# Optimization experiments

Measured on AMD Instinct MI355X. Metric: run time of the kernel, lower is better.

Reference implementation:

```python
import jax, jax.numpy as jnp
import numpy as np

N, H, DK, DV, DFF, D = 2, 8, 32, 32, 512, 256
B, S = 2, 2048
MASK_VALUE = -1e-30
EPS = 1e-14  # K.epsilon()**2 with default epsilon 1e-7


def glorot(key, shape):
    fan_in, fan_out = shape[-2], shape[-1]
    limit = np.sqrt(6.0 / (fan_in + fan_out))
    return jax.random.uniform(key, shape, jnp.float32, -limit, limit)


def setup_inputs() -> dict:
    key = jax.random.key(0)
    ks = jax.random.split(key, 8)
    return {
        "x": jax.random.normal(ks[0], (B, S, D), jnp.float32),
        "mask": jnp.ones((B, S), jnp.float32),
        "Wq": glorot(ks[1], (N, H, D, DK)),
        "Wk": glorot(ks[2], (N, H, D, DK)),
        "Wv": glorot(ks[3], (N, H, D, DV)),
        "Wo": glorot(ks[4], (N, H * DV, D)),
        "W1": glorot(ks[5], (N, D, DFF)),
        "b1": jnp.zeros((N, DFF), jnp.float32),
        "W2": glorot(ks[6], (N, DFF, D)),
        "b2": jnp.zeros((N, D), jnp.float32),
        "gamma": jnp.ones((2 * N,), jnp.float32),
        "beta": jnp.zeros((2 * N,), jnp.float32),
    }


def _layernorm(x, g, b):
    mean = jnp.mean(x, axis=-1, keepdims=True)
    var = jnp.mean(jnp.square(x - mean), axis=-1, keepdims=True)
    return (x - mean) / jnp.sqrt(var + EPS) * g + b


def reference(x, mask, Wq, Wk, Wv, Wo, W1, b1, W2, b2, gamma, beta):
    m = mask[:, None, None, :]  # [B,1,1,S], multiplies score rows' key axis
    for i in range(N):
        # batched multi-head attention (no 1/sqrt(dk) scaling, faithful to source)
        q = jnp.einsum("bsd,hdk->bhsk", x, Wq[i])
        k = jnp.einsum("bsd,hdk->bhsk", x, Wk[i])
        v = jnp.einsum("bsd,hdv->bhsv", x, Wv[i])
        A = jnp.einsum("bhsk,bhtk->bhst", q, k)  # [B,H,S,S]
        A = m * A + (1.0 - m) * MASK_VALUE
        A = jax.nn.softmax(A, axis=-1)
        o = jnp.einsum("bhst,bhtv->bhsv", A, v)
        conc = o.transpose(0, 2, 1, 3).reshape(x.shape[0], x.shape[1], H * DV)
        x = x + conc @ Wo[i]
        x = _layernorm(x, gamma[2 * i], beta[2 * i])
        ffn = jax.nn.relu(x @ W1[i] + b1[i]) @ W2[i] + b2[i]
        x = x + ffn
        x = _layernorm(x, gamma[2 * i + 1], beta[2 * i + 1])
    return x
```

## Files before the change

### kernel.cpp

```cpp
#include <hip/hip_runtime.h>
#include <hip/hip_bf16.h>

#define NL 2
#define NH 8
#define DKk 32
#define DVv 32
#define DFF 512
#define DD 256
#define BB 2
#define SS 2048
#define MROWS (BB*SS)
#define MASK_VALUE (-1e-30f)
#define LN_EPS 1e-14f
#define L2E 1.4426950408889634f
#define SOFT_SHIFT_L2E (50.0f*L2E)

typedef __hip_bfloat16 bf16;
typedef unsigned short us;
typedef short bf16x8 __attribute__((ext_vector_type(8)));
typedef float f32x4  __attribute__((ext_vector_type(4)));
typedef unsigned short us4 __attribute__((ext_vector_type(4)));

#define O_XF   256
#define O_QB   (O_XF+1048576)
#define O_KH   (O_QB+1048576)
#define O_KL   (O_KH+524288)
#define O_VT   (O_KL+524288)
#define O_XH   (O_VT+524288)
#define O_XL   (O_XH+524288)
#define O_OP   (O_XL+524288)
#define O_ML   (O_OP+2097152)
#define O_MASK (O_ML+65536)
#define O_WQ   (O_MASK+4096)
#define O_WK   (O_WQ+131072)
#define O_WV   (O_WK+131072)
#define O_WO   (O_WV+131072)
#define O_W1   (O_WO+131072)
#define O_B1   (O_W1+262144)
#define O_W2   (O_B1+1024)
#define O_B2   (O_W2+262144)
#define O_GM   (O_B2+512)
#define O_BT   (O_GM+4)
#define O_PREP (O_BT+4)
#define CONV_TOTAL (1048576+4096+131072+131072+131072+131072+262144+1024+262144+512+4+4)
#define CONV_BLOCKS ((CONV_TOTAL+255)/256)
#define PQH 0u
#define PQL 393216u
#define POH 786432u
#define POL 917504u
#define P1H 1048576u
#define P1L 1310720u
#define P2H 1572864u
#define P2L 1835008u

__device__ __forceinline__ float us2f(us u){
  unsigned int v = ((unsigned int)u) << 16; float f;
  __builtin_memcpy(&f, &v, 4); return f;
}
__device__ __forceinline__ us f2bf_rne(float f){
  unsigned int b = __float_as_uint(f);
  b += 0x7FFFu + ((b>>16)&1u);
  return (us)(b>>16);
}

#if __has_builtin(__builtin_amdgcn_exp2f)
#define EXP2F(x) __builtin_amdgcn_exp2f(x)
#else
#define EXP2F(x) exp2f(x)
#endif

#if __has_builtin(__builtin_amdgcn_cvt_pk_bf16_f32)
typedef __bf16 bf16x2_t __attribute__((ext_vector_type(2)));
__device__ __forceinline__ int pack_bf16(float a, float b){
  bf16x2_t r = __builtin_amdgcn_cvt_pk_bf16_f32(a, b);
  int i; __builtin_memcpy(&i, &r, 4); return i;
}
#else
__device__ __forceinline__ int pack_bf16(float a, float b){
  int b0 = __float_as_int(a) + 0x8000;
  int b1 = __float_as_int(b) + 0x8000;
  return (b1 & 0xFFFF0000) | ((int)((unsigned)b0 >> 16));
}
#endif

__device__ __forceinline__ void gl_lds16(const us* g, us* l){
  __builtin_amdgcn_global_load_lds(
    (const __attribute__((address_space(1))) unsigned int*)g,
    (__attribute__((address_space(3))) unsigned int*)l, 16, 0, 0);
}

__device__ __forceinline__ size_t xhl_idx(int row, int col){
  int rt = row>>6, rg = (row>>4)&3, L15 = row&15;
  int kc = col>>5, Q = (col>>3)&3, j = col&7;
  return ((size_t)(rt*8+kc))*2048 + rg*512 + Q*128 + L15*8 + j;
}

__global__ void detect_kernel(const us* __restrict__ x, int n, int* __restrict__ flagp){
  __shared__ int bad;
  if(threadIdx.x==0) bad = 0;
  __syncthreads();
  int lim = n < 4096 ? n : 4096;
  int mybad = 0;
  for(int i=threadIdx.x; i<lim; i+=256){
    float f = us2f(x[i]);
    if(!(fabsf(f) < 1e3f)) mybad = 1;
  }
  if(mybad) atomicOr(&bad, 1);
  __syncthreads();
  if(threadIdx.x==0) *flagp = bad ? 1 : 0;
}

__device__ __forceinline__ float conv1(const void* src, int i, int flag){
  if(flag) return ((const float*)src)[i];
  return us2f(((const us*)src)[i]);
}

__global__ void mega_conv(const void* s0, const void* s1, const void* s2, const void* s3,
                          const void* s4, const void* s5, const void* s6, const void* s7,
                          const void* s8, const void* s9, const void* s10, const void* s11,
                          float* __restrict__ ws, const int* __restrict__ flagp)
{
  int g = blockIdx.x*256 + threadIdx.x;
  int flag = *flagp;
  if(g < 1048576){
    float v = conv1(s0, g, flag);
    ws[O_XF+g] = v;
    us hb = f2bf_rne(v);
    us lb = f2bf_rne(v - us2f(hb));
    size_t xi = xhl_idx(g>>8, g&255);
    ((us*)(ws+O_XH))[xi] = hb;
    ((us*)(ws+O_XL))[xi] = lb;
    return;
  }
  g -= 1048576;
  if(g < 4096){ ws[O_MASK+g] = conv1(s1, g, flag)*L2E; return; }
  g -= 4096;
  if(g < 131072){ ws[O_WQ+g] = conv1(s2, g, flag); return; }
  g -= 131072;
  if(g < 131072){ ws[O_WK+g] = conv1(s3, g, flag); return; }
  g -= 131072;
  if(g < 131072){ ws[O_WV+g] = conv1(s4, g, flag); return; }
  g -= 131072;
  if(g < 131072){ ws[O_WO+g] = conv1(s5, g, flag); return; }
  g -= 131072;
  if(g < 262144){ ws[O_W1+g] = conv1(s6, g, flag); return; }
  g -= 262144;
  if(g < 1024){ ws[O_B1+g] = conv1(s7, g, flag); return; }
  g -= 1024;
  if(g < 262144){ ws[O_W2+g] = conv1(s8, g, flag); return; }
  g -= 262144;
  if(g < 512){ ws[O_B2+g] = conv1(s9, g, flag); return; }
  g -= 512;
  if(g < 4){ ws[O_GM+g] = conv1(s10, g, flag); return; }
  g -= 4;
  if(g < 4){ ws[O_BT+g] = conv1(s11, g, flag); return; }
}

__device__ __forceinline__ void prep_b(const float* W0, const float* W1, const float* W2,
                                       us* Bh, us* Bl, int Kd, int Nd, int qkv, int g)
{
  int total = (Kd/32)*(Nd/16)*64;
  if(g >= total) return;
  int lane = g & 63, fi = g >> 6;
  int ncN = Nd/16;
  int nc = fi % ncN, kc = fi / ncN;
  int Q = lane>>4, L15 = lane&15;
  int n = nc*16 + L15;
  const float* src;
  int stride;
  if(qkv){
    int sec = n>>8, h = (n>>5)&7, kq = n&31;
    const float* Wp = (sec==0)?W0:((sec==1)?W1:W2);
    src = Wp + (size_t)h*256*32 + kq;
    stride = 32;
  } else {
    src = W0 + n;
    stride = Nd;
  }
  #pragma unroll
  for(int j=0;j<8;j++){
    int k = kc*32 + Q*8 + j;
    float v = src[(size_t)k*stride];
    us hb = f2bf_rne(v);
    Bh[(size_t)g*8 + j] = hb;
    Bl[(size_t)g*8 + j] = f2bf_rne(v - us2f(hb));
  }
}

__global__ void mega_prep(float* __restrict__ ws)
{
  int gb = blockIdx.x;
  int layer = gb >> 8, lb = gb & 255;
  us* prep = (us*)(ws + O_PREP);
  const float* Wq = ws + O_WQ + layer*65536;
  const float* Wk = ws + O_WK + layer*65536;
  const float* Wv = ws + O_WV + layer*65536;
  const float* Wo = ws + O_WO + layer*65536;
  const float* W1 = ws + O_W1 + layer*131072;
  const float* W2 = ws + O_W2 + layer*131072;
  if(lb < 96){
    int g = lb*256 + threadIdx.x;
    prep_b(Wq, Wk, Wv, prep+PQH+(size_t)layer*196608, prep+PQL+(size_t)layer*196608, 256, 768, 1, g);
  } else if(lb < 128){
    int g = (lb-96)*256 + threadIdx.x;
    prep_b(Wo, nullptr, nullptr, prep+POH+(size_t)layer*65536, prep+POL+(size_t)layer*65536, 256, 256, 0, g);
  } else if(lb < 192){
    int g = (lb-128)*256 + threadIdx.x;
    prep_b(W1, nullptr, nullptr, prep+P1H+(size_t)layer*131072, prep+P1L+(size_t)layer*131072, 256, 512, 0, g);
  } else {
    int g = (lb-192)*256 + threadIdx.x;
    prep_b(W2, nullptr, nullptr, prep+P2H+(size_t)layer*131072, prep+P2L+(size_t)layer*131072, 512, 256, 0, g);
  }
}

template<int MODE, int ASRC>
__launch_bounds__(256)
__global__ void gemm_mfma(const float* __restrict__ A,
                          const us* __restrict__ Axh, const us* __restrict__ Axl,
                          const float* __restrict__ OpartA, const float* __restrict__ MLA,
                          const us* __restrict__ Bh, const us* __restrict__ Bl,
                          const float* __restrict__ bias, const float* __restrict__ res,
                          float* __restrict__ O,
                          us* __restrict__ QH, us* __restrict__ QL,
                          us* __restrict__ KH, us* __restrict__ KL, us* __restrict__ VT,
                          int Ncols, int Kdim)
{
  __shared__ __align__(16) us Ah[2048], Al[2048];
  __shared__ __align__(16) us Bhs[2048], Bls[2048];
  const int t = threadIdx.x;
  const int w = t>>6, lane = t&63;
  const int Q = lane>>4, L15 = lane&15;
  const int row0 = blockIdx.x*64;
  const int nc0 = blockIdx.y*4;
  const int col0 = blockIdx.y*64;

  f32x4 acc[2][2];
  #pragma unroll
  for(int i=0;i<2;i++)
    #pragma unroll
    for(int j=0;j<2;j++) acc[i][j] = (f32x4){0.f,0.f,0.f,0.f};

  const int r1 = t>>3;
  const int kl = (t&7)*4;
  const int Qc = kl>>3, j0 = kl&7;
  const int nKc = Kdim>>5;
  const int ncW = Ncols>>4;

  for(int kc=0; kc<nKc; kc++){
    if(ASRC==1){
      size_t abase = ((size_t)(blockIdx.x*nKc + kc))*2048;
      gl_lds16(&Axh[abase + (size_t)t*8], &Ah[t*8]);
      gl_lds16(&Axl[abase + (size_t)t*8], &Al[t*8]);
    } else {
      #pragma unroll
      for(int half=0; half<2; half++){
        int r = r1 + half*32;
        int rg = r>>4, L = r&15;
        float4 v;
        if(ASRC==2){
          int row = row0 + r;
          int b_ = row>>11, s_ = row&2047;
          size_t i0 = (size_t)(b_*8 + kc)*2048 + s_;
          float l = MLA[i0] + MLA[i0 + 32768];
          float inv = 1.f/l;
          float4 o0 = *(const float4*)&OpartA[i0*32 + kl];
          float4 o1 = *(const float4*)&OpartA[(i0+32768)*32 + kl];
          v.x=(o0.x+o1.x)*inv; v.y=(o0.y+o1.y)*inv;
          v.z=(o0.z+o1.z)*inv; v.w=(o0.w+o1.w)*inv;
        } else {
          v = *(const float4*)&A[(size_t)(row0+r)*Kdim + kc*32 + kl];
        }
        float f[4] = {v.x, v.y, v.z, v.w};
        us4 h4, l4;
        #pragma unroll
        for(int j=0;j<4;j++){
          us hb = f2bf_rne(f[j]);
          h4[j] = hb; l4[j] = f2bf_rne(f[j] - us2f(hb));
        }
        int off = (rg*4+Qc)*128 + L*8 + j0;
        *(us4*)&Ah[off] = h4;
        *(us4*)&Al[off] = l4;
      }
    }
    {
      size_t gidx = ((size_t)(kc*ncW + nc0 + w)*64 + lane)*8;
      gl_lds16(&Bh[gidx], &Bhs[t*8]);
      gl_lds16(&Bl[gidx], &Bls[t*8]);
    }
    __syncthreads();

    bf16x8 aAh[2], aAl[2], bBh[2], bBl[2];
    #pragma unroll
    for(int rg2=0;rg2<2;rg2++){
      int rg = (w&1)*2 + rg2;
      aAh[rg2] = *(const bf16x8*)&Ah[rg*512 + lane*8];
      aAl[rg2] = *(const bf16x8*)&Al[rg*512 + lane*8];
    }
    #pragma unroll
    for(int cg2=0;cg2<2;cg2++){
      int nc = (w>>1)*2 + cg2;
      bBh[cg2] = *(const bf16x8*)&Bhs[nc*512 + lane*8];
      bBl[cg2] = *(const bf16x8*)&Bls[nc*512 + lane*8];
    }
    #pragma unroll
    for(int rg2=0;rg2<2;rg2++)
      #pragma unroll
      for(int cg2=0;cg2<2;cg2++){
        acc[rg2][cg2] = __builtin_amdgcn_mfma_f32_16x16x32_bf16(aAl[rg2], bBh[cg2], acc[rg2][cg2], 0,0,0);
        acc[rg2][cg2] = __builtin_amdgcn_mfma_f32_16x16x32_bf16(aAh[rg2], bBl[cg2], acc[rg2][cg2], 0,0,0);
        acc[rg2][cg2] = __builtin_amdgcn_mfma_f32_16x16x32_bf16(aAh[rg2], bBh[cg2], acc[rg2][cg2], 0,0,0);
      }
    __syncthreads();
  }

  #pragma unroll
  for(int rg2=0;rg2<2;rg2++)
    #pragma unroll
    for(int cg2=0;cg2<2;cg2++)
      #pragma unroll
      for(int r=0;r<4;r++){
        int row = row0 + (w&1)*32 + rg2*16 + Q*4 + r;
        int c   = col0 + (w>>1)*32 + cg2*16 + L15;
        float va = acc[rg2][cg2][r];
        if(MODE==0){
          int b_ = row>>11, s_ = row&2047;
          int sec = c>>8, h = (c>>5)&7, kq = c&31;
          int bh = b_*NH + h;
          size_t idx = ((size_t)(bh*128 + (s_>>4))*64 + (kq>>3)*16 + (s_&15))*8 + (kq&7);
          if(sec==0){
            us hb = f2bf_rne(va);
            QH[idx] = hb; QL[idx] = f2bf_rne(va - us2f(hb));
          } else if(sec==1){
            us hb = f2bf_rne(va);
            KH[idx] = hb; KL[idx] = f2bf_rne(va - us2f(hb));
          } else {
            size_t vidx = ((size_t)((bh*64 + (s_>>5))*2 + (kq>>4))*64 + ((s_&31)>>3)*16 + (kq&15))*8 + (s_&7);
            VT[vidx] = f2bf_rne(va);
          }
        } else if(MODE==1){
          O[(size_t)row*Ncols + c] = res[(size_t)row*Ncols + c] + va;
        } else if(MODE==2){
          float v = va + bias[c];
          O[(size_t)row*Ncols + c] = v>0.f ? v : 0.f;
        } else {
          O[(size_t)row*Ncols + c] = res[(size_t)row*Ncols + c] + va + bias[c];
        }
      }
}

__launch_bounds__(256)
__global__ void attn_kernel(const us* __restrict__ QH, const us* __restrict__ QL,
                            const us* __restrict__ KH, const us* __restrict__ KL,
                            const us* __restrict__ VT,
                            const float* __restrict__ mask,
                            float* __restrict__ Opart, float* __restrict__ ML)
{
  __shared__ __align__(16) us Khs[4096], Kls[4096], Vts[4096];
  __shared__ __align__(16) float Msl[128];
  const int t = threadIdx.x;
  const int bh = blockIdx.x >> 6;
  const int qt = (blockIdx.x & 63) >> 1;
  const int ks = blockIdx.x & 1;
  const int b_ = bh >> 3;
  const int wv = t >> 6;
  const int lane = t & 63;
  const int Q = lane >> 4, L15 = lane & 15;
  const int q0 = qt*64 + wv*16;

  size_t qidx = ((size_t)(bh*128 + qt*4 + wv)*64 + lane)*8;
  const bf16x8 qh_v = *(const bf16x8*)&QH[qidx];
  const bf16x8 ql_v = *(const bf16x8*)&QL[qidx];

  const us* KHbh = KH + (size_t)bh*65536;
  const us* KLbh = KL + (size_t)bh*65536;
  const us* VTbh = VT + (size_t)bh*65536;

  f32x4 Oa0a = {0.f,0.f,0.f,0.f}, Oa0b = {0.f,0.f,0.f,0.f};
  f32x4 Oa1a = {0.f,0.f,0.f,0.f}, Oa1b = {0.f,0.f,0.f,0.f};
  float lacc = 0.f;

  const int kend = ks*1024 + 1024;
  for(int t0 = ks*1024; t0 < kend; t0 += 128){
    {
      size_t kbase = (size_t)(t0>>4)*512;
      size_t vbase = (size_t)(t0>>5)*1024;
      #pragma unroll
      for(int ii=0; ii<2; ii++){
        int s = t + ii*256;
        gl_lds16(&KHbh[kbase + (size_t)s*8], &Khs[s*8]);
        gl_lds16(&KLbh[kbase + (size_t)s*8], &Kls[s*8]);
        gl_lds16(&VTbh[vbase + (size_t)s*8], &Vts[s*8]);
      }
      if(t < 128) Msl[t] = mask[b_*SS + t0 + t];
    }
    __syncthreads();

    f32x4 St[8];
    const f32x4 zz = {0.f,0.f,0.f,0.f};
    #pragma unroll
    for(int kt=0;kt<8;kt++){
      bf16x8 aKh = *(const bf16x8*)&Khs[kt*512 + lane*8];
      bf16x8 aKl = *(const bf16x8*)&Kls[kt*512 + lane*8];
      f32x4 a = __builtin_amdgcn_mfma_f32_16x16x32_bf16(aKl, qh_v, zz, 0,0,0);
      a = __builtin_amdgcn_mfma_f32_16x16x32_bf16(aKh, ql_v, a, 0,0,0);
      a = __builtin_amdgcn_mfma_f32_16x16x32_bf16(aKh, qh_v, a, 0,0,0);
      St[kt] = a;
    }

    float lsum = 0.f;
    #pragma unroll
    for(int kt=0;kt<8;kt++){
      float4 mv = *(const float4*)&Msl[kt*16 + Q*4];
      float mvr[4] = {mv.x, mv.y, mv.z, mv.w};
      #pragma unroll
      for(int r=0;r<4;r++){
        float p = EXP2F(fmaf(mvr[r], St[kt][r], -SOFT_SHIFT_L2E));
        St[kt][r] = p;
        lsum += p;
      }
    }
    lacc += lsum;

    int pk[8][2];
    #pragma unroll
    for(int kt=0;kt<8;kt++){
      pk[kt][0] = pack_bf16(St[kt][0], St[kt][1]);
      pk[kt][1] = pack_bf16(St[kt][2], St[kt][3]);
    }

    #pragma unroll
    for(int c=0;c<4;c++){
      union { int i[4]; bf16x8 v; } bu;
      #pragma unroll
      for(int d=0;d<4;d++){
        int srcl = (((Q&1)*2 + (d>>1))<<4) | L15;
        int vlo = __shfl(pk[2*c  ][d&1], srcl, 64);
        int vhi = __shfl(pk[2*c+1][d&1], srcl, 64);
        bu.i[d] = (Q & 2) ? vhi : vlo;
      }
      bf16x8 aV0 = *(const bf16x8*)&Vts[(c*2+0)*512 + lane*8];
      bf16x8 aV1 = *(const bf16x8*)&Vts[(c*2+1)*512 + lane*8];
      if(c < 2){
        Oa0a = __builtin_amdgcn_mfma_f32_16x16x32_bf16(aV0, bu.v, Oa0a, 0,0,0);
        Oa1a = __builtin_amdgcn_mfma_f32_16x16x32_bf16(aV1, bu.v, Oa1a, 0,0,0);
      } else {
        Oa0b = __builtin_amdgcn_mfma_f32_16x16x32_bf16(aV0, bu.v, Oa0b, 0,0,0);
        Oa1b = __builtin_amdgcn_mfma_f32_16x16x32_bf16(aV1, bu.v, Oa1b, 0,0,0);
      }
    }
    __syncthreads();
  }

  f32x4 Oa0 = Oa0a + Oa0b;
  f32x4 Oa1 = Oa1a + Oa1b;
  lacc += __shfl_xor(lacc, 16);
  lacc += __shfl_xor(lacc, 32);

  float* opp = &Opart[((size_t)(ks*16+bh)*SS + q0 + L15)*32];
  #pragma unroll
  for(int r=0;r<4;r++){
    opp[Q*4+r]    = Oa0[r];
    opp[16+Q*4+r] = Oa1[r];
  }
  if(Q==0){
    ML[(size_t)(ks*16+bh)*SS + q0 + L15] = lacc;
  }
}

__launch_bounds__(256)
__global__ void ln_kernel(float* __restrict__ xf, const float* __restrict__ gamma,
                          const float* __restrict__ beta, int gi,
                          us* __restrict__ xh, us* __restrict__ xl,
                          void* __restrict__ out, int write_out,
                          const int* __restrict__ flagp)
{
  __shared__ float s1[4], s2[4];
  const int r = blockIdx.x;
  const int t = threadIdx.x;
  float v = xf[(size_t)r*DD + t];
  float sum = v, sumsq = v*v;
  #pragma unroll
  for(int off=1; off<64; off<<=1){
    sum   += __shfl_xor(sum, off);
    sumsq += __shfl_xor(sumsq, off);
  }
  if((t&63)==0){ s1[t>>6]=sum; s2[t>>6]=sumsq; }
  __syncthreads();
  float tot  = s1[0]+s1[1]+s1[2]+s1[3];
  float tot2 = s2[0]+s2[1]+s2[2]+s2[3];
  float mean = tot*(1.f/DD);
  float var  = tot2*(1.f/DD) - mean*mean;
  float g = gamma[gi], bb = beta[gi];
  float val = (v-mean)*rsqrtf(var+LN_EPS)*g + bb;
  xf[(size_t)r*DD + t] = val;
  us hb = f2bf_rne(val);
  us lb = f2bf_rne(val - us2f(hb));
  size_t xi = xhl_idx(r, t);
  xh[xi] = hb; xl[xi] = lb;
  if(write_out){
    if(*flagp) ((float*)out)[(size_t)r*DD + t] = val;
    else       ((bf16*)out)[(size_t)r*DD + t] = __float2bfloat16(val);
  }
}

extern "C" void kernel_launch(void* const* d_in, const int* in_sizes, int n_in,
                              void* d_out, int out_size, void* d_ws, size_t ws_size,
                              hipStream_t stream)
{
  float* ws = (float*)d_ws;
  int* flagp = (int*)d_ws;

  float* xf  = ws + O_XF;
  us* QHb = (us*)(ws + O_QB);
  us* QLb = QHb + 1048576;
  us* KH = (us*)(ws + O_KH);
  us* KL = (us*)(ws + O_KL);
  us* VT = (us*)(ws + O_VT);
  us* XH = (us*)(ws + O_XH);
  us* XL = (us*)(ws + O_XL);
  float* Opart = ws + O_OP;
  float* ML  = ws + O_ML;
  float* fh  = Opart;
  float* maskf = ws + O_MASK;
  float* b1f = ws + O_B1;
  float* b2f_ = ws + O_B2;
  float* gmf = ws + O_GM;
  float* btf = ws + O_BT;
  us* prep = (us*)(ws + O_PREP);

  detect_kernel<<<1,256,0,stream>>>((const us*)d_in[0], in_sizes[0], flagp);
  mega_conv<<<CONV_BLOCKS,256,0,stream>>>(d_in[0], d_in[1], d_in[2], d_in[3], d_in[4], d_in[5],
                                          d_in[6], d_in[7], d_in[8], d_in[9], d_in[10], d_in[11],
                                          ws, flagp);
  mega_prep<<<512,256,0,stream>>>(ws);

  for(int i=0;i<NL;i++){
    const float* b1i = b1f + (size_t)i*DFF;
    const float* b2i = b2f_ + (size_t)i*DD;

    dim3 g0(64, 12);
    gemm_mfma<0,1><<<g0,256,0,stream>>>(nullptr, XH, XL, nullptr, nullptr,
                                        prep+PQH+(size_t)i*196608, prep+PQL+(size_t)i*196608,
                                        nullptr, nullptr, nullptr,
                                        QHb, QLb, KH, KL, VT, 768, 256);
    attn_kernel<<<1024,256,0,stream>>>(QHb, QLb, KH, KL, VT, maskf, Opart, ML);
    dim3 g1(64, 4);
    gemm_mfma<1,2><<<g1,256,0,stream>>>(nullptr, nullptr, nullptr, Opart, ML,
                                        prep+POH+(size_t)i*65536, prep+POL+(size_t)i*65536,
                                        nullptr, xf, xf,
                                        nullptr, nullptr, nullptr, nullptr, nullptr, 256, 256);
    ln_kernel<<<MROWS,256,0,stream>>>(xf, gmf, btf, 2*i, XH, XL, d_out, 0, flagp);
    dim3 g2(64, 8);
    gemm_mfma<2,1><<<g2,256,0,stream>>>(nullptr, XH, XL, nullptr, nullptr,
                                        prep+P1H+(size_t)i*131072, prep+P1L+(size_t)i*131072,
                                        b1i, nullptr, fh,
                                        nullptr, nullptr, nullptr, nullptr, nullptr, 512, 256);
    dim3 g3(64, 4);
    gemm_mfma<3,0><<<g3,256,0,stream>>>(fh, nullptr, nullptr, nullptr, nullptr,
                                        prep+P2H+(size_t)i*131072, prep+P2L+(size_t)i*131072,
                                        b2i, xf, xf,
                                        nullptr, nullptr, nullptr, nullptr, nullptr, 256, 512);
    ln_kernel<<<MROWS,256,0,stream>>>(xf, gmf, btf, 2*i+1, XH, XL, d_out, (i==NL-1)?1:0, flagp);
  }
}
```

Measured before the change: 281.3 us.

## Fuse weight conversion into prep kernel and widen GEMM tiles for QKV/FFN1

Weight conversion and bf16 hi/lo splitting now read the raw input weights directly inside one combined conv_prep kernel. This drops the intermediate fp32 weight copies in the workspace and saves one kernel launch. The QKV and FFN1 GEMMs move to a new gemm_mfma_w kernel with 64x128 tiles, where each wave computes 4x2 MFMA fragments. That gives more reuse of the A tile and halves the grid's column blocks, at the cost of fewer blocks and more registers per thread.

```diff
diff --git a/kernel.cpp b/kernel.cpp
--- a/kernel.cpp
+++ b/kernel.cpp
@@ -10,7 +10,6 @@
 #define BB 2
 #define SS 2048
 #define MROWS (BB*SS)
-#define MASK_VALUE (-1e-30f)
 #define LN_EPS 1e-14f
 #define L2E 1.4426950408889634f
 #define SOFT_SHIFT_L2E (50.0f*L2E)
@@ -31,19 +30,14 @@
 #define O_OP   (O_XL+524288)
 #define O_ML   (O_OP+2097152)
 #define O_MASK (O_ML+65536)
-#define O_WQ   (O_MASK+4096)
-#define O_WK   (O_WQ+131072)
-#define O_WV   (O_WK+131072)
-#define O_WO   (O_WV+131072)
-#define O_W1   (O_WO+131072)
-#define O_B1   (O_W1+262144)
-#define O_W2   (O_B1+1024)
-#define O_B2   (O_W2+262144)
+#define O_B1   (O_MASK+4096)
+#define O_B2   (O_B1+1024)
 #define O_GM   (O_B2+512)
 #define O_BT   (O_GM+4)
 #define O_PREP (O_BT+4)
-#define CONV_TOTAL (1048576+4096+131072+131072+131072+131072+262144+1024+262144+512+4+4)
+#define CONV_TOTAL (1048576+4096+1024+512+4+4)
 #define CONV_BLOCKS ((CONV_TOTAL+255)/256)
+#define PREP_BLOCKS 512
 #define PQH 0u
 #define PQL 393216u
 #define POH 786432u
@@ -110,18 +104,74 @@
   if(threadIdx.x==0) *flagp = bad ? 1 : 0;
 }
 
-__device__ __forceinline__ float conv1(const void* src, int i, int flag){
+__device__ __forceinline__ float conv1(const void* src, size_t i, int flag){
   if(flag) return ((const float*)src)[i];
   return us2f(((const us*)src)[i]);
 }
 
-__global__ void mega_conv(const void* s0, const void* s1, const void* s2, const void* s3,
-                          const void* s4, const void* s5, const void* s6, const void* s7,
-                          const void* s8, const void* s9, const void* s10, const void* s11,
+__device__ __forceinline__ void prep_b_raw(const void* W0, const void* W1v, const void* W2v,
+                                           int baseoff, us* __restrict__ Bh, us* __restrict__ Bl,
+                                           int Kd, int Nd, int qkv, int g, int flag)
+{
+  int total = (Kd/32)*(Nd/16)*64;
+  if(g >= total) return;
+  int lane = g & 63, fi = g >> 6;
+  int ncN = Nd/16;
+  int nc = fi % ncN, kc = fi / ncN;
+  int Q = lane>>4, L15 = lane&15;
+  int n = nc*16 + L15;
+  const void* src;
+  int off0, stride;
+  if(qkv){
+    int sec = n>>8, h = (n>>5)&7, kq = n&31;
+    src = (sec==0)?W0:((sec==1)?W1v:W2v);
+    off0 = baseoff + h*8192 + kq;
+    stride = 32;
+  } else {
+    src = W0;
+    off0 = baseoff + n;
+    stride = Nd;
+  }
+  #pragma unroll
+  for(int j=0;j<8;j++){
+    int k = kc*32 + Q*8 + j;
+    float v = conv1(src, (size_t)off0 + (size_t)k*stride, flag);
+    us hb = f2bf_rne(v);
+    Bh[(size_t)g*8 + j] = hb;
+    Bl[(size_t)g*8 + j] = f2bf_rne(v - us2f(hb));
+  }
+}
+
+__global__ void conv_prep(const void* s0, const void* s1, const void* sWq, const void* sWk,
+                          const void* sWv, const void* sWo, const void* sW1, const void* sb1,
+                          const void* sW2, const void* sb2, const void* sgm, const void* sbt,
                           float* __restrict__ ws, const int* __restrict__ flagp)
 {
-  int g = blockIdx.x*256 + threadIdx.x;
   int flag = *flagp;
+  int b = blockIdx.x;
+  if(b < PREP_BLOCKS){
+    int layer = b >> 8, lb = b & 255;
+    us* prep = (us*)(ws + O_PREP);
+    if(lb < 96){
+      int g = lb*256 + threadIdx.x;
+      prep_b_raw(sWq, sWk, sWv, layer*65536, prep+PQH+(size_t)layer*196608,
+                 prep+PQL+(size_t)layer*196608, 256, 768, 1, g, flag);
+    } else if(lb < 128){
+      int g = (lb-96)*256 + threadIdx.x;
+      prep_b_raw(sWo, nullptr, nullptr, layer*65536, prep+POH+(size_t)layer*65536,
+                 prep+POL+(size_t)layer*65536, 256, 256, 0, g, flag);
+    } else if(lb < 192){
+      int g = (lb-128)*256 + threadIdx.x;
+      prep_b_raw(sW1, nullptr, nullptr, layer*131072, prep+P1H+(size_t)layer*131072,
+                 prep+P1L+(size_t)layer*131072, 256, 512, 0, g, flag);
+    } else {
+      int g = (lb-192)*256 + threadIdx.x;
+      prep_b_raw(sW2, nullptr, nullptr, layer*131072, prep+P2H+(size_t)layer*131072,
+                 prep+P2L+(size_t)layer*131072, 512, 256, 0, g, flag);
+    }
+    return;
+  }
+  int g = (b - PREP_BLOCKS)*256 + threadIdx.x;
   if(g < 1048576){
     float v = conv1(s0, g, flag);
     ws[O_XF+g] = v;
@@ -135,94 +185,119 @@
   g -= 1048576;
   if(g < 4096){ ws[O_MASK+g] = conv1(s1, g, flag)*L2E; return; }
   g -= 4096;
-  if(g < 131072){ ws[O_WQ+g] = conv1(s2, g, flag); return; }
-  g -= 131072;
-  if(g < 131072){ ws[O_WK+g] = conv1(s3, g, flag); return; }
-  g -= 131072;
-  if(g < 131072){ ws[O_WV+g] = conv1(s4, g, flag); return; }
-  g -= 131072;
-  if(g < 131072){ ws[O_WO+g] = conv1(s5, g, flag); return; }
-  g -= 131072;
-  if(g < 262144){ ws[O_W1+g] = conv1(s6, g, flag); return; }
-  g -= 262144;
-  if(g < 1024){ ws[O_B1+g] = conv1(s7, g, flag); return; }
+  if(g < 1024){ ws[O_B1+g] = conv1(sb1, g, flag); return; }
   g -= 1024;
-  if(g < 262144){ ws[O_W2+g] = conv1(s8, g, flag); return; }
-  g -= 262144;
-  if(g < 512){ ws[O_B2+g] = conv1(s9, g, flag); return; }
+  if(g < 512){ ws[O_B2+g] = conv1(sb2, g, flag); return; }
   g -= 512;
-  if(g < 4){ ws[O_GM+g] = conv1(s10, g, flag); return; }
+  if(g < 4){ ws[O_GM+g] = conv1(sgm, g, flag); return; }
   g -= 4;
-  if(g < 4){ ws[O_BT+g] = conv1(s11, g, flag); return; }
-}
-
-__device__ __forceinline__ void prep_b(const float* W0, const float* W1, const float* W2,
-                                       us* Bh, us* Bl, int Kd, int Nd, int qkv, int g)
+  if(g < 4){ ws[O_BT+g] = conv1(sbt, g, flag); return; }
+}
+
+template<int MODE>
+__launch_bounds__(256)
+__global__ void gemm_mfma_w(const us* __restrict__ Axh, const us* __restrict__ Axl,
+                            const us* __restrict__ Bh, const us* __restrict__ Bl,
+                            const float* __restrict__ bias,
+                            float* __restrict__ O,
+                            us* __restrict__ QH, us* __restrict__ QL,
+                            us* __restrict__ KH, us* __restrict__ KL, us* __restrict__ VT,
+                            int Ncols, int Kdim)
 {
-  int total = (Kd/32)*(Nd/16)*64;
-  if(g >= total) return;
-  int lane = g & 63, fi = g >> 6;
-  int ncN = Nd/16;
-  int nc = fi % ncN, kc = fi / ncN;
-  int Q = lane>>4, L15 = lane&15;
-  int n = nc*16 + L15;
-  const float* src;
-  int stride;
-  if(qkv){
-    int sec = n>>8, h = (n>>5)&7, kq = n&31;
-    const float* Wp = (sec==0)?W0:((sec==1)?W1:W2);
-    src = Wp + (size_t)h*256*32 + kq;
-    stride = 32;
-  } else {
-    src = W0 + n;
-    stride = Nd;
-  }
+  __shared__ __align__(16) us Ah[2048], Al[2048];
+  __shared__ __align__(16) us Bhs[4096], Bls[4096];
+  const int t = threadIdx.x;
+  const int w = t>>6, lane = t&63;
+  const int Q = lane>>4, L15 = lane&15;
+  const int row0 = blockIdx.x*64;
+  const int nc0 = blockIdx.y*8;
+  const int col0 = blockIdx.y*128;
+
+  f32x4 acc[4][2];
   #pragma unroll
-  for(int j=0;j<8;j++){
-    int k = kc*32 + Q*8 + j;
-    float v = src[(size_t)k*stride];
-    us hb = f2bf_rne(v);
-    Bh[(size_t)g*8 + j] = hb;
-    Bl[(size_t)g*8 + j] = f2bf_rne(v - us2f(hb));
-  }
-}
-
-__global__ void mega_prep(float* __restrict__ ws)
-{
-  int gb = blockIdx.x;
-  int layer = gb >> 8, lb = gb & 255;
-  us* prep = (us*)(ws + O_PREP);
-  const float* Wq = ws + O_WQ + layer*65536;
-  const float* Wk = ws + O_WK + layer*65536;
-  const float* Wv = ws + O_WV + layer*65536;
-  const float* Wo = ws + O_WO + layer*65536;
-  const float* W1 = ws + O_W1 + layer*131072;
-  const float* W2 = ws + O_W2 + layer*131072;
-  if(lb < 96){
-    int g = lb*256 + threadIdx.x;
-    prep_b(Wq, Wk, Wv, prep+PQH+(size_t)layer*196608, prep+PQL+(size_t)layer*196608, 256, 768, 1, g);
-  } else if(lb < 128){
-    int g = (lb-96)*256 + threadIdx.x;
-    prep_b(Wo, nullptr, nullptr, prep+POH+(size_t)layer*65536, prep+POL+(size_t)layer*65536, 256, 256, 0, g);
-  } else if(lb < 192){
-    int g = (lb-128)*256 + threadIdx.x;
-    prep_b(W1, nullptr, nullptr, prep+P1H+(size_t)layer*131072, prep+P1L+(size_t)layer*131072, 256, 512, 0, g);
-  } else {
-    int g = (lb-192)*256 + threadIdx.x;
-    prep_b(W2, nullptr, nullptr, prep+P2H+(size_t)layer*131072, prep+P2L+(size_t)layer*131072, 512, 256, 0, g);
-  }
+  for(int i=0;i<4;i++)
+    #pragma unroll
+    for(int j=0;j<2;j++) acc[i][j] = (f32x4){0.f,0.f,0.f,0.f};
+
+  const int nKc = Kdim>>5;
+  const int ncW = Ncols>>4;
+
+  for(int kc=0; kc<nKc; kc++){
+    {
+      size_t abase = ((size_t)(blockIdx.x*nKc + kc))*2048;
+      gl_lds16(&Axh[abase + (size_t)t*8], &Ah[t*8]);
+      gl_lds16(&Axl[abase + (size_t)t*8], &Al[t*8]);
+      #pragma unroll
+      for(int ii=0; ii<2; ii++){
+        int unit = w + ii*4;
+        size_t gidx = ((size_t)(kc*ncW + nc0 + unit)*64 + lane)*8;
+        gl_lds16(&Bh[gidx], &Bhs[unit*512 + lane*8]);
+        gl_lds16(&Bl[gidx], &Bls[unit*512 + lane*8]);
+      }
+    }
+    __syncthreads();
+
+    bf16x8 aAh[4], aAl[4], bBh[2], bBl[2];
+    #pragma unroll
+    for(int rg=0;rg<4;rg++){
+      aAh[rg] = *(const bf16x8*)&Ah[rg*512 + lane*8];
+      aAl[rg] = *(const bf16x8*)&Al[rg*512 + lane*8];
+    }
+    #pragma unroll
+    for(int cg2=0;cg2<2;cg2++){
+      int unit = w*2 + cg2;
+      bBh[cg2] = *(const bf16x8*)&Bhs[unit*512 + lane*8];
+      bBl[cg2] = *(const bf16x8*)&Bls[unit*512 + lane*8];
+    }
+    #pragma unroll
+    for(int rg=0;rg<4;rg++)
+      #pragma unroll
+      for(int cg2=0;cg2<2;cg2++){
+        acc[rg][cg2] = __builtin_amdgcn_mfma_f32_16x16x32_bf16(aAl[rg], bBh[cg2], acc[rg][cg2], 0,0,0);
+        acc[rg][cg2] = __builtin_amdgcn_mfma_f32_16x16x32_bf16(aAh[rg], bBl[cg2], acc[rg][cg2], 0,0,0);
+        acc[rg][cg2] = __builtin_amdgcn_mfma_f32_16x16x32_bf16(aAh[rg], bBh[cg2], acc[rg][cg2], 0,0,0);
+      }
+    __syncthreads();
+  }
+
+  #pragma unroll
+  for(int rg=0;rg<4;rg++)
+    #pragma unroll
+    for(int cg2=0;cg2<2;cg2++)
+      #pragma unroll
+      for(int r=0;r<4;r++){
+        int row = row0 + rg*16 + Q*4 + r;
+        int c   = col0 + w*32 + cg2*16 + L15;
+        float va = acc[rg][cg2][r];
+        if(MODE==0){
+          int b_ = row>>11, s_ = row&2047;
+          int sec = c>>8, h = (c>>5)&7, kq = c&31;
+          int bh = b_*NH + h;
+          size_t idx = ((size_t)(bh*128 + (s_>>4))*64 + (kq>>3)*16 + (s_&15))*8 + (kq&7);
+          if(sec==0){
+            us hb = f2bf_rne(va);
+            QH[idx] = hb; QL[idx] = f2bf_rne(va - us2f(hb));
+          } else if(sec==1){
+            us hb = f2bf_rne(va);
+            KH[idx] = hb; KL[idx] = f2bf_rne(va - us2f(hb));
+          } else {
+            size_t vidx = ((size_t)((bh*64 + (s_>>5))*2 + (kq>>4))*64 + ((s_&31)>>3)*16 + (kq&15))*8 + (s_&7);
+            VT[vidx] = f2bf_rne(va);
+          }
+        } else {
+          float v = va + bias[c];
+          O[(size_t)row*Ncols + c] = v>0.f ? v : 0.f;
+        }
+      }
 }
 
 template<int MODE, int ASRC>
 __launch_bounds__(256)
 __global__ void gemm_mfma(const float* __restrict__ A,
-                          const us* __restrict__ Axh, const us* __restrict__ Axl,
                           const float* __restrict__ OpartA, const float* __restrict__ MLA,
                           const us* __restrict__ Bh, const us* __restrict__ Bl,
                           const float* __restrict__ bias, const float* __restrict__ res,
                           float* __restrict__ O,
-                          us* __restrict__ QH, us* __restrict__ QL,
-                          us* __restrict__ KH, us* __restrict__ KL, us* __restrict__ VT,
                           int Ncols, int Kdim)
 {
   __shared__ __align__(16) us Ah[2048], Al[2048];
@@ -247,11 +322,7 @@
   const int ncW = Ncols>>4;
 
   for(int kc=0; kc<nKc; kc++){
-    if(ASRC==1){
-      size_t abase = ((size_t)(blockIdx.x*nKc + kc))*2048;
-      gl_lds16(&Axh[abase + (size_t)t*8], &Ah[t*8]);
-      gl_lds16(&Axl[abase + (size_t)t*8], &Al[t*8]);
-    } else {
+    {
       #pragma unroll
       for(int half=0; half<2; half++){
         int r = r1 + half*32;
@@ -322,26 +393,8 @@
         int row = row0 + (w&1)*32 + rg2*16 + Q*4 + r;
         int c   = col0 + (w>>1)*32 + cg2*16 + L15;
         float va = acc[rg2][cg2][r];
-        if(MODE==0){
-          int b_ = row>>11, s_ = row&2047;
-          int sec = c>>8, h = (c>>5)&7, kq = c&31;
-          int bh = b_*NH + h;
-          size_t idx = ((size_t)(bh*128 + (s_>>4))*64 + (kq>>3)*16 + (s_&15))*8 + (kq&7);
-          if(sec==0){
-            us hb = f2bf_rne(va);
-            QH[idx] = hb; QL[idx] = f2bf_rne(va - us2f(hb));
-          } else if(sec==1){
-            us hb = f2bf_rne(va);
-            KH[idx] = hb; KL[idx] = f2bf_rne(va - us2f(hb));
-          } else {
-            size_t vidx = ((size_t)((bh*64 + (s_>>5))*2 + (kq>>4))*64 + ((s_&31)>>3)*16 + (kq&15))*8 + (s_&7);
-            VT[vidx] = f2bf_rne(va);
-          }
-        } else if(MODE==1){
+        if(MODE==1){
           O[(size_t)row*Ncols + c] = res[(size_t)row*Ncols + c] + va;
-        } else if(MODE==2){
-          float v = va + bias[c];
-          O[(size_t)row*Ncols + c] = v>0.f ? v : 0.f;
         } else {
           O[(size_t)row*Ncols + c] = res[(size_t)row*Ncols + c] + va + bias[c];
         }
@@ -521,7 +574,6 @@
   float* Opart = ws + O_OP;
   float* ML  = ws + O_ML;
   float* fh  = Opart;
-  float* maskf = ws + O_MASK;
   float* b1f = ws + O_B1;
   float* b2f_ = ws + O_B2;
   float* gmf = ws + O_GM;
@@ -529,37 +581,35 @@
   us* prep = (us*)(ws + O_PREP);
 
   detect_kernel<<<1,256,0,stream>>>((const us*)d_in[0], in_sizes[0], flagp);
-  mega_conv<<<CONV_BLOCKS,256,0,stream>>>(d_in[0], d_in[1], d_in[2], d_in[3], d_in[4], d_in[5],
-                                          d_in[6], d_in[7], d_in[8], d_in[9], d_in[10], d_in[11],
-                                          ws, flagp);
-  mega_prep<<<512,256,0,stream>>>(ws);
+  conv_prep<<<PREP_BLOCKS+CONV_BLOCKS,256,0,stream>>>(
+      d_in[0], d_in[1], d_in[2], d_in[3], d_in[4], d_in[5],
+      d_in[6], d_in[7], d_in[8], d_in[9], d_in[10], d_in[11],
+      ws, flagp);
 
   for(int i=0;i<NL;i++){
     const float* b1i = b1f + (size_t)i*DFF;
     const float* b2i = b2f_ + (size_t)i*DD;
 
-    dim3 g0(64, 12);
-    gemm_mfma<0,1><<<g0,256,0,stream>>>(nullptr, XH, XL, nullptr, nullptr,
+    dim3 g0(64, 6);
+    gemm_mfma_w<0><<<g0,256,0,stream>>>(XH, XL,
                                         prep+PQH+(size_t)i*196608, prep+PQL+(size_t)i*196608,
-                                        nullptr, nullptr, nullptr,
+                                        nullptr, nullptr,
                                         QHb, QLb, KH, KL, VT, 768, 256);
-    attn_kernel<<<1024,256,0,stream>>>(QHb, QLb, KH, KL, VT, maskf, Opart, ML);
+    attn_kernel<<<1024,256,0,stream>>>(QHb, QLb, KH, KL, VT, ws + O_MASK, Opart, ML);
     dim3 g1(64, 4);
-    gemm_mfma<1,2><<<g1,256,0,stream>>>(nullptr, nullptr, nullptr, Opart, ML,
+    gemm_mfma<1,2><<<g1,256,0,stream>>>(nullptr, Opart, ML,
                                         prep+POH+(size_t)i*65536, prep+POL+(size_t)i*65536,
-                                        nullptr, xf, xf,
-                                        nullptr, nullptr, nullptr, nullptr, nullptr, 256, 256);
+                                        nullptr, xf, xf, 256, 256);
     ln_kernel<<<MROWS,256,0,stream>>>(xf, gmf, btf, 2*i, XH, XL, d_out, 0, flagp);
-    dim3 g2(64, 8);
-    gemm_mfma<2,1><<<g2,256,0,stream>>>(nullptr, XH, XL, nullptr, nullptr,
+    dim3 g2(64, 4);
+    gemm_mfma_w<2><<<g2,256,0,stream>>>(XH, XL,
                                         prep+P1H+(size_t)i*131072, prep+P1L+(size_t)i*131072,
-                                        b1i, nullptr, fh,
+                                        b1i, fh,
                                         nullptr, nullptr, nullptr, nullptr, nullptr, 512, 256);
     dim3 g3(64, 4);
-    gemm_mfma<3,0><<<g3,256,0,stream>>>(fh, nullptr, nullptr, nullptr, nullptr,
+    gemm_mfma<3,0><<<g3,256,0,stream>>>(fh, nullptr, nullptr,
                                         prep+P2H+(size_t)i*131072, prep+P2L+(size_t)i*131072,
-                                        b2i, xf, xf,
-                                        nullptr, nullptr, nullptr, nullptr, nullptr, 256, 512);
+                                        b2i, xf, xf, 256, 512);
     ln_kernel<<<MROWS,256,0,stream>>>(xf, gmf, btf, 2*i+1, XH, XL, d_out, (i==NL-1)?1:0, flagp);
   }
 }
```

New measurement: 287.8 us. +2.3%, slower.
